# Performance work log

Measured on AMD Instinct MI355X. Metric: run time of the kernel, lower is better.

## Reference

```python
import jax, jax.numpy as jnp
import numpy as np

N = 100000        # nodes
E_RAND = 1600000  # random edges (self loops appended -> E = E_RAND + N)
H = 64            # agg_hidden
IN = 7            # in_channels
L = 3             # n_layer
FC = 128          # fc_hidden
C = 2             # num_classes
G = 256           # graphs in the batch
SLOPE = 0.2       # GATv2 LeakyReLU negative slope


def _gatv2(x, src, dst, Wl, bl, Wr, br, att, bias):
    # GATv2Conv, heads=1, concat=True, no edge_attr
    xl = x @ Wl.T + bl                                      # [N,H] source transform
    xr = x @ Wr.T + br                                      # [N,H] target transform
    e = jax.nn.leaky_relu(xl[src] + xr[dst], SLOPE) @ att   # [E] per-edge score
    m = jax.ops.segment_max(e, dst, num_segments=N)         # segment softmax over in-edges
    w = jnp.exp(e - m[dst])
    denom = jax.ops.segment_sum(w, dst, num_segments=N)
    alpha = w / denom[dst]                                  # self loops guarantee denom > 0
    out = jax.ops.segment_sum(alpha[:, None] * xl[src], dst, num_segments=N)
    return out + bias


def _forward(x, eps, m0, v0, mrest, vrest, fc1_W, fc1_b, fc2_W, fc2_b, edge_index, batch):
    src, dst = edge_index[0], edge_index[1]
    mean = jax.nn.elu(_gatv2(x, src, dst, *m0))
    log_var = jax.nn.elu(_gatv2(x, src, dst, *v0))
    for i in range(L - 1):  # dropout is a no-op in eval mode
        mean = jax.nn.elu(_gatv2(mean, src, dst, *[p[i] for p in mrest]))
        log_var = jax.nn.elu(_gatv2(log_var, src, dst, *[p[i] for p in vrest]))
    z = mean + eps * jnp.exp(0.5 * log_var)                 # reparameterize
    counts = jax.ops.segment_sum(jnp.ones((N,), z.dtype), batch, num_segments=G)
    zg = jax.ops.segment_sum(z, batch, num_segments=G) / counts[:, None]  # global_mean_pool
    h = jax.nn.relu(zg @ fc1_W.T + fc1_b)
    logits = h @ fc2_W.T + fc2_b
    return jax.nn.log_softmax(logits, axis=1), mean, log_var


def setup_inputs() -> dict:
    key = jax.random.key(0)
    ks = iter(jax.random.split(key, 48))

    def nrm(shape, s=0.1):
        return s * jax.random.normal(next(ks), shape, jnp.float32)

    x = jax.random.normal(next(ks), (N, IN), jnp.float32)
    src = jax.random.randint(next(ks), (E_RAND,), 0, N)
    dst = jax.random.randint(next(ks), (E_RAND,), 0, N)
    loops = jnp.arange(N)
    edge_index = jnp.stack([jnp.concatenate([src, loops]),
                            jnp.concatenate([dst, loops])])  # add_self_loops=True
    batch = jnp.sort(jax.random.randint(next(ks), (N,), 0, G))
    eps = jax.random.normal(next(ks), (N, H), jnp.float32)

    d = dict(x=x, eps=eps, edge_index=edge_index, batch=batch)
    for pre, din in (("m0", IN), ("v0", IN)):
        d[pre + "_Wl"] = nrm((H, din)); d[pre + "_bl"] = nrm((H,))
        d[pre + "_Wr"] = nrm((H, din)); d[pre + "_br"] = nrm((H,))
        d[pre + "_att"] = nrm((H,));    d[pre + "_bias"] = nrm((H,))
    for pre in ("m", "v"):  # stacked hidden layers [L-1, ...]
        d[pre + "_Wl"] = nrm((L - 1, H, H)); d[pre + "_bl"] = nrm((L - 1, H))
        d[pre + "_Wr"] = nrm((L - 1, H, H)); d[pre + "_br"] = nrm((L - 1, H))
        d[pre + "_att"] = nrm((L - 1, H));   d[pre + "_bias"] = nrm((L - 1, H))
    d["fc1_W"] = nrm((FC, H)); d["fc1_b"] = nrm((FC,))
    d["fc2_W"] = nrm((C, FC)); d["fc2_b"] = nrm((C,))
    return d


def reference(x, eps, edge_index, batch,
              m0_Wl, m0_bl, m0_Wr, m0_br, m0_att, m0_bias,
              v0_Wl, v0_bl, v0_Wr, v0_br, v0_att, v0_bias,
              m_Wl, m_bl, m_Wr, m_br, m_att, m_bias,
              v_Wl, v_bl, v_Wr, v_br, v_att, v_bias,
              fc1_W, fc1_b, fc2_W, fc2_b):
    m0 = (m0_Wl, m0_bl, m0_Wr, m0_br, m0_att, m0_bias)
    v0 = (v0_Wl, v0_bl, v0_Wr, v0_br, v0_att, v0_bias)
    mrest = (m_Wl, m_bl, m_Wr, m_br, m_att, m_bias)
    vrest = (v_Wl, v_bl, v_Wr, v_br, v_att, v_bias)
    return _forward(x, eps, m0, v0, mrest, vrest, fc1_W, fc1_b, fc2_W, fc2_b, edge_index, batch)
```

## Files before the change

### kernel.cpp

```cpp
#include <hip/hip_runtime.h>
#include <hip/hip_fp16.h>
#include <math.h>


#define BSH 7
#define BMSK ((1 << BSH) - 1)
#define CHUNK 4096
#define SNB 4096

typedef _Float16 h2 __attribute__((ext_vector_type(2)));
typedef _Float16 h8 __attribute__((ext_vector_type(8)));
typedef float f4 __attribute__((ext_vector_type(4)));

__device__ __forceinline__ float elu1(float v) {
    return v > 0.f ? v : (__expf(v) - 1.f);
}

__device__ __forceinline__ float exp2fast(float x) {
#if defined(__has_builtin)
#if __has_builtin(__builtin_amdgcn_exp2f)
    return __builtin_amdgcn_exp2f(x);
#else
    return exp2f(x);
#endif
#else
    return exp2f(x);
#endif
}

__device__ __forceinline__ float dot2f(h2 a, h2 b, float c) {
#if defined(__has_builtin)
#if __has_builtin(__builtin_amdgcn_fdot2)
    return __builtin_amdgcn_fdot2(a, b, c, false);
#else
    return fmaf((float)a.x, (float)b.x, fmaf((float)a.y, (float)b.y, c));
#endif
#else
    return fmaf((float)a.x, (float)b.x, fmaf((float)a.y, (float)b.y, c));
#endif
}

template <int CTRL>
__device__ __forceinline__ float dppf(float v) {
    int r = __builtin_amdgcn_update_dpp(0, __builtin_bit_cast(int, v), CTRL, 0xF, 0xF, true);
    return __builtin_bit_cast(float, r);
}


__global__ void k_hist_bucket(const int* __restrict__ dst, int E,
                              int* __restrict__ bcnt, int nbk) {
    __shared__ int h[1024];
    for (int i = threadIdx.x; i < 1024; i += blockDim.x) h[i] = 0;
    __syncthreads();
    int stride = gridDim.x * blockDim.x;
    for (int e = blockIdx.x * blockDim.x + threadIdx.x; e < E; e += stride)
        atomicAdd(&h[dst[e] >> BSH], 1);
    __syncthreads();
    for (int i = threadIdx.x; i < nbk; i += blockDim.x)
        if (h[i]) atomicAdd(&bcnt[i], h[i]);
}

__global__ void k_scan_buckets(const int* __restrict__ bcnt, int nbk, int* __restrict__ boff) {
    __shared__ int sh[1024];
    int t = threadIdx.x;
    int v = (t < nbk) ? bcnt[t] : 0;
    sh[t] = v;
    __syncthreads();
    for (int o = 1; o < 1024; o <<= 1) {
        int u = (t >= o) ? sh[t - o] : 0;
        __syncthreads();
        sh[t] += u;
        __syncthreads();
    }
    if (t < nbk) boff[t] = sh[t] - v;
    if (t == nbk - 1) boff[nbk] = sh[t];
}

__global__ __launch_bounds__(256) void k_binfill(
    const int* __restrict__ src, const int* __restrict__ dst, int E,
    const int* __restrict__ boff, int* __restrict__ bfill, int* __restrict__ pairs) {
    __shared__ int h[1024];
    __shared__ int sbase[1024];
    int c0 = blockIdx.x * CHUNK;
    int c1 = min(c0 + CHUNK, E);
    for (int i = threadIdx.x; i < 1024; i += 256) h[i] = 0;
    __syncthreads();
    for (int e = c0 + threadIdx.x; e < c1; e += 256)
        atomicAdd(&h[dst[e] >> BSH], 1);
    __syncthreads();
    for (int i = threadIdx.x; i < 1024; i += 256) {
        int c = h[i];
        sbase[i] = c ? (boff[i] + atomicAdd(&bfill[i], c)) : 0;
        h[i] = 0;
    }
    __syncthreads();
    for (int e = c0 + threadIdx.x; e < c1; e += 256) {
        int d = dst[e];
        int b = d >> BSH;
        int off = atomicAdd(&h[b], 1);
        pairs[sbase[b] + off] = (src[e] << BSH) | (d & BMSK);
    }
}

__global__ __launch_bounds__(256) void k_bucket_csr(
    const int* __restrict__ pairs, const int* __restrict__ boff,
    int* __restrict__ rowptr, int* __restrict__ col, int N, int E) {
    __shared__ int deg[128], fill[128], scan[128], base[128];
    int b = blockIdx.x;
    int e0 = boff[b], e1 = boff[b + 1];
    int t = threadIdx.x;
    if (t < 128) { deg[t] = 0; fill[t] = 0; }
    __syncthreads();
    for (int i = e0 + t; i < e1; i += 256)
        atomicAdd(&deg[pairs[i] & BMSK], 1);
    __syncthreads();
    if (t < 128) scan[t] = deg[t];
    __syncthreads();
    for (int o = 1; o < 128; o <<= 1) {
        int u = (t >= o && t < 128) ? scan[t - o] : 0;
        __syncthreads();
        if (t < 128) scan[t] += u;
        __syncthreads();
    }
    if (t < 128) {
        int excl = e0 + scan[t] - deg[t];
        int node = (b << BSH) + t;
        if (node < N) rowptr[node] = excl;
        if (node == N - 1) rowptr[N] = E;
        base[t] = excl;
    }
    __syncthreads();
    for (int i = e0 + t; i < e1; i += 256) {
        int pk = pairs[i];
        int d = pk & BMSK;
        int pos = base[d] + atomicAdd(&fill[d], 1);
        col[pos] = ((unsigned)pk) >> BSH;
    }
}


__global__ __launch_bounds__(256) void k_deg_hist(const int* __restrict__ rowptr, int n,
                                                  int* __restrict__ bin_cnt,
                                                  int* __restrict__ blk_base) {
    __shared__ int h[256];
    h[threadIdx.x] = 0;
    __syncthreads();
    int b0 = blockIdx.x * SNB;
    int b1 = min(b0 + SNB, n);
    for (int i = b0 + threadIdx.x; i < b1; i += 256) {
        int d = 255 - min(rowptr[i + 1] - rowptr[i], 255);
        atomicAdd(&h[d], 1);
    }
    __syncthreads();
    int c = h[threadIdx.x];
    blk_base[blockIdx.x * 256 + threadIdx.x] = c ? atomicAdd(&bin_cnt[threadIdx.x], c) : 0;
}

__global__ void k_scan256(const int* __restrict__ bin_cnt, int* __restrict__ bin_off) {
    __shared__ int sh[256];
    int t = threadIdx.x;
    int v = bin_cnt[t];
    sh[t] = v;
    __syncthreads();
    for (int o = 1; o < 256; o <<= 1) {
        int u = (t >= o) ? sh[t - o] : 0;
        __syncthreads();
        sh[t] += u;
        __syncthreads();
    }
    bin_off[t] = sh[t] - v;
}

__global__ __launch_bounds__(256) void k_deg_scatter(const int* __restrict__ rowptr, int n,
                                                     const int* __restrict__ bin_off,
                                                     const int* __restrict__ blk_base,
                                                     int* __restrict__ nodeof) {
    __shared__ int h[256];
    h[threadIdx.x] = 0;
    __syncthreads();
    int b0 = blockIdx.x * SNB;
    int b1 = min(b0 + SNB, n);
    for (int i = b0 + threadIdx.x; i < b1; i += 256) {
        int d = 255 - min(rowptr[i + 1] - rowptr[i], 255);
        int my = atomicAdd(&h[d], 1);
        nodeof[bin_off[d] + blk_base[blockIdx.x * 256 + d] + my] = i;
    }
}


__global__ void k_transform7(const float* __restrict__ X,
                             const float* __restrict__ mWl, const float* __restrict__ mbl,
                             const float* __restrict__ mWr, const float* __restrict__ mbr,
                             const float* __restrict__ vWl, const float* __restrict__ vbl,
                             const float* __restrict__ vWr, const float* __restrict__ vbr,
                             __half* __restrict__ xlb, __half* __restrict__ xrb, int n) {
    int t = blockIdx.x * blockDim.x + threadIdx.x;
    int node = t >> 6;
    if (node >= n) return;
    int h = t & 63;
    float aml = mbl[h], amr = mbr[h], avl = vbl[h], avr = vbr[h];
#pragma unroll
    for (int k = 0; k < 7; ++k) {
        float xv = X[node * 7 + k];
        aml = fmaf(xv, mWl[h * 7 + k], aml);
        amr = fmaf(xv, mWr[h * 7 + k], amr);
        avl = fmaf(xv, vWl[h * 7 + k], avl);
        avr = fmaf(xv, vWr[h * 7 + k], avr);
    }
    size_t o = (size_t)node * 128;
    xlb[o + h] = __float2half(aml);
    xlb[o + 64 + h] = __float2half(avl);
    xrb[o + h] = __float2half(amr);
    xrb[o + 64 + h] = __float2half(avr);
}

__global__ __launch_bounds__(256) void k_transform_mfma2(
    const float* __restrict__ Xm, const float* __restrict__ Xv,
    const float* __restrict__ mWl, const float* __restrict__ mbl,
    const float* __restrict__ mWr, const float* __restrict__ mbr,
    const float* __restrict__ vWl, const float* __restrict__ vbl,
    const float* __restrict__ vWr, const float* __restrict__ vbr,
    __half* __restrict__ xlb, __half* __restrict__ xrb, int n) {
    int brn = blockIdx.y;
    const float* X  = brn ? Xv : Xm;
    const float* Wl = brn ? vWl : mWl;
    const float* bl = brn ? vbl : mbl;
    const float* Wr = brn ? vWr : mWr;
    const float* br = brn ? vbr : mbr;
    int base = brn * 64;

    __shared__ float biasLds[128];
    {
        int t = threadIdx.x;
        if (t < 64) biasLds[t] = bl[t];
        else if (t < 128) biasLds[t] = br[t - 64];
    }
    __syncthreads();
    int lane = threadIdx.x & 63;
    int l16 = lane & 15, lhi = lane >> 4;

    h8 aW[2][8];
    const float* Wp0 = Wl + (size_t)l16 * 64 + lhi * 8;
    const float* Wp1 = Wr + (size_t)l16 * 64 + lhi * 8;
#pragma unroll
    for (int tl = 0; tl < 4; ++tl) {
#pragma unroll
        for (int c = 0; c < 2; ++c) {
            const float* p0 = Wp0 + (size_t)tl * 16 * 64 + c * 32;
            const float* p1 = Wp1 + (size_t)tl * 16 * 64 + c * 32;
            float4 u0 = *(const float4*)p0, u1 = *(const float4*)(p0 + 4);
            float4 v0 = *(const float4*)p1, v1 = *(const float4*)(p1 + 4);
            h8 a0 = {(_Float16)u0.x, (_Float16)u0.y, (_Float16)u0.z, (_Float16)u0.w,
                     (_Float16)u1.x, (_Float16)u1.y, (_Float16)u1.z, (_Float16)u1.w};
            h8 a1 = {(_Float16)v0.x, (_Float16)v0.y, (_Float16)v0.z, (_Float16)v0.w,
                     (_Float16)v1.x, (_Float16)v1.y, (_Float16)v1.z, (_Float16)v1.w};
            aW[0][tl * 2 + c] = a0;
            aW[1][tl * 2 + c] = a1;
        }
    }

    int ntiles = (n + 15) >> 4;
    int wtile = blockIdx.x * 4 + (threadIdx.x >> 6);
    int wstride = gridDim.x * 4;
    for (int tile = wtile; tile < ntiles; tile += wstride) {
        int nb = tile * 16;
        int node = nb + l16;
        int nload = min(node, n - 1);
        h8 Bf[2];
#pragma unroll
        for (int c = 0; c < 2; ++c) {
            const float* p = X + (size_t)nload * 64 + c * 32 + lhi * 8;
            float4 u0 = *(const float4*)p, u1 = *(const float4*)(p + 4);
            h8 b = {(_Float16)u0.x, (_Float16)u0.y, (_Float16)u0.z, (_Float16)u0.w,
                    (_Float16)u1.x, (_Float16)u1.y, (_Float16)u1.z, (_Float16)u1.w};
            Bf[c] = b;
        }
        f4 acc[2][4];
#pragma unroll
        for (int m = 0; m < 2; ++m)
#pragma unroll
            for (int tl = 0; tl < 4; ++tl) {
                f4 a = {0.f, 0.f, 0.f, 0.f};
                a = __builtin_amdgcn_mfma_f32_16x16x32_f16(aW[m][tl * 2 + 0], Bf[0], a, 0, 0, 0);
                a = __builtin_amdgcn_mfma_f32_16x16x32_f16(aW[m][tl * 2 + 1], Bf[1], a, 0, 0, 0);
                acc[m][tl] = a;
            }
        if (node < n) {
#pragma unroll
            for (int m = 0; m < 2; ++m) {
                __half* op = (m ? xrb : xlb) + (size_t)node * 128 + base;
#pragma unroll
                for (int tl = 0; tl < 4; ++tl) {
                    float4 bb = *(const float4*)&biasLds[m * 64 + tl * 16 + 4 * lhi];
                    h2 lo = {(_Float16)(acc[m][tl][0] + bb.x), (_Float16)(acc[m][tl][1] + bb.y)};
                    h2 hi = {(_Float16)(acc[m][tl][2] + bb.z), (_Float16)(acc[m][tl][3] + bb.w)};
                    uint2 pk = {*(unsigned*)&lo, *(unsigned*)&hi};
                    *(uint2*)(op + tl * 16 + 4 * lhi) = pk;
                }
            }
        }
    }
}


__global__ __launch_bounds__(256) void k_aggregate2(
    const __half* __restrict__ xlb, const __half* __restrict__ xrb,
    const float* __restrict__ attm, const float* __restrict__ attv,
    const float* __restrict__ biasm, const float* __restrict__ biasv,
    const int* __restrict__ rowptr, const int* __restrict__ col,
    const int* __restrict__ nodeof,
    float* __restrict__ outm, float* __restrict__ outv, int n) {
    int t = blockIdx.x * blockDim.x + threadIdx.x;
    int gid = t >> 4;
    if (gid >= n) return;
    int node = nodeof[gid];
    int l = t & 15;
    int s = l & 7;
    bool isv = l >= 8;

    int4 xri = ((const int4*)(xrb + (size_t)node * 128))[l];
    h2 xr0 = *(h2*)&xri.x, xr1 = *(h2*)&xri.y, xr2 = *(h2*)&xri.z, xr3 = *(h2*)&xri.w;
    const float* ap = (isv ? attv : attm) + s * 8;
    float4 af0 = *(const float4*)ap, af1 = *(const float4*)(ap + 4);
    const float C6 = 0.6f * 1.44269504f;
    const float C4 = 0.4f * 1.44269504f;
    h2 a6_0 = {(_Float16)(af0.x * C6), (_Float16)(af0.y * C6)};
    h2 a6_1 = {(_Float16)(af0.z * C6), (_Float16)(af0.w * C6)};
    h2 a6_2 = {(_Float16)(af1.x * C6), (_Float16)(af1.y * C6)};
    h2 a6_3 = {(_Float16)(af1.z * C6), (_Float16)(af1.w * C6)};
    h2 a4_0 = {(_Float16)(af0.x * C4), (_Float16)(af0.y * C4)};
    h2 a4_1 = {(_Float16)(af0.z * C4), (_Float16)(af0.w * C4)};
    h2 a4_2 = {(_Float16)(af1.x * C4), (_Float16)(af1.y * C4)};
    h2 a4_3 = {(_Float16)(af1.z * C4), (_Float16)(af1.w * C4)};

    float ac0 = 0.f, ac1 = 0.f, ac2 = 0.f, ac3 = 0.f;
    float ac4 = 0.f, ac5 = 0.f, ac6 = 0.f, ac7 = 0.f;
    float ssum = 0.f;

    auto proc = [&](int4 qi) {
        h2 x0 = *(h2*)&qi.x, x1 = *(h2*)&qi.y, x2 = *(h2*)&qi.z, x3 = *(h2*)&qi.w;
        h2 y0 = x0 + xr0, y1 = x1 + xr1, y2 = x2 + xr2, y3 = x3 + xr3;
        int z0i = (*(int*)&y0) & 0x7FFF7FFF;
        int z1i = (*(int*)&y1) & 0x7FFF7FFF;
        int z2i = (*(int*)&y2) & 0x7FFF7FFF;
        int z3i = (*(int*)&y3) & 0x7FFF7FFF;
        h2 z0 = *(h2*)&z0i, z1 = *(h2*)&z1i, z2 = *(h2*)&z2i, z3 = *(h2*)&z3i;
        float sc = dot2f(y0, a6_0, 0.f);
        float sa = dot2f(z0, a4_0, 0.f);
        sc = dot2f(y1, a6_1, sc);
        sa = dot2f(z1, a4_1, sa);
        sc = dot2f(y2, a6_2, sc);
        sa = dot2f(z2, a4_2, sa);
        sc = dot2f(y3, a6_3, sc);
        sa = dot2f(z3, a4_3, sa);
        sc += sa;
        sc += dppf<0xB1>(sc);
        sc += dppf<0x4E>(sc);
        sc += dppf<0x141>(sc);
        float w = exp2fast(sc);
        ssum += w;
        ac0 = fmaf(w, (float)x0.x, ac0);
        ac1 = fmaf(w, (float)x0.y, ac1);
        ac2 = fmaf(w, (float)x1.x, ac2);
        ac3 = fmaf(w, (float)x1.y, ac3);
        ac4 = fmaf(w, (float)x2.x, ac4);
        ac5 = fmaf(w, (float)x2.y, ac5);
        ac6 = fmaf(w, (float)x3.x, ac6);
        ac7 = fmaf(w, (float)x3.y, ac7);
    };

    int r0 = rowptr[node], r1 = rowptr[node + 1];
    const int4* xp = (const int4*)xlb + l;
    int last = r1 - 1;
    int nb = (r1 - r0) >> 2;
    int e = r0;
    int t0 = 0, t1 = 0, t2 = 0, t3 = 0;
    int4 qA0, qA1, qA2, qA3;
    if (nb) {
        int s0 = col[e], s1 = col[e + 1], s2 = col[e + 2], s3 = col[e + 3];
        qA0 = xp[(size_t)s0 * 16]; qA1 = xp[(size_t)s1 * 16];
        qA2 = xp[(size_t)s2 * 16]; qA3 = xp[(size_t)s3 * 16];
        int p = e + 4;
        t0 = col[min(p, last)];     t1 = col[min(p + 1, last)];
        t2 = col[min(p + 2, last)]; t3 = col[min(p + 3, last)];
    }
    for (int b = 0; b < nb; ++b) {
        int4 qB0, qB1, qB2, qB3;
        bool more = (b + 1 < nb);
        if (more) {
            qB0 = xp[(size_t)t0 * 16]; qB1 = xp[(size_t)t1 * 16];
            qB2 = xp[(size_t)t2 * 16]; qB3 = xp[(size_t)t3 * 16];
            int p = e + 8;
            t0 = col[min(p, last)];     t1 = col[min(p + 1, last)];
            t2 = col[min(p + 2, last)]; t3 = col[min(p + 3, last)];
        }
        proc(qA0); proc(qA1); proc(qA2); proc(qA3);
        if (more) { qA0 = qB0; qA1 = qB1; qA2 = qB2; qA3 = qB3; }
        e += 4;
    }
    for (e = r0 + nb * 4; e < r1; ++e)
        proc(xp[(size_t)col[e] * 16]);

    float inv = 1.f / ssum;
    const float* bp = (isv ? biasv : biasm) + s * 8;
    float4 b0 = *(const float4*)bp, b1 = *(const float4*)(bp + 4);
    float* op = (isv ? outv : outm) + (size_t)node * 64 + s * 8;
    float4 r0v, r1v;
    r0v.x = elu1(fmaf(ac0, inv, b0.x));
    r0v.y = elu1(fmaf(ac1, inv, b0.y));
    r0v.z = elu1(fmaf(ac2, inv, b0.z));
    r0v.w = elu1(fmaf(ac3, inv, b0.w));
    r1v.x = elu1(fmaf(ac4, inv, b1.x));
    r1v.y = elu1(fmaf(ac5, inv, b1.y));
    r1v.z = elu1(fmaf(ac6, inv, b1.z));
    r1v.w = elu1(fmaf(ac7, inv, b1.w));
    *(float4*)op = r0v;
    *(float4*)(op + 4) = r1v;
}


__global__ void k_zpool(const float* __restrict__ mean, const float* __restrict__ logvar,
                        const float* __restrict__ eps, const int* __restrict__ batch,
                        float* __restrict__ zsum, float* __restrict__ cnt, int n) {
    int wave = blockIdx.x * 4 + (threadIdx.x >> 6);
    int lane = threadIdx.x & 63;
    int n0 = wave * 16;
    if (n0 >= n) return;
    int n1 = min(n0 + 16, n);
    float acc = 0.f, c = 0.f;
    int gcur = -1;
    for (int nd = n0; nd < n1; ++nd) {
        int g = batch[nd];
        if (g != gcur) {
            if (gcur >= 0) {
                atomicAdd(&zsum[gcur * 64 + lane], acc);
                if (lane == 0) atomicAdd(&cnt[gcur], c);
            }
            gcur = g; acc = 0.f; c = 0.f;
        }
        size_t o = (size_t)nd * 64 + lane;
        float z = fmaf(eps[o], __expf(0.5f * logvar[o]), mean[o]);
        acc += z;
        c += 1.f;
    }
    if (gcur >= 0) {
        atomicAdd(&zsum[gcur * 64 + lane], acc);
        if (lane == 0) atomicAdd(&cnt[gcur], c);
    }
}


__global__ void k_fchead(const float* __restrict__ zsum, const float* __restrict__ cnt,
                         const float* __restrict__ fc1W, const float* __restrict__ fc1b,
                         const float* __restrict__ fc2W, const float* __restrict__ fc2b,
                         float* __restrict__ out) {
    __shared__ float zg[64];
    __shared__ float h1[128];
    __shared__ float lg[2];
    int g = blockIdx.x;
    int t = threadIdx.x;
    if (t < 64) zg[t] = zsum[g * 64 + t] / cnt[g];
    __syncthreads();
    float h = fc1b[t];
#pragma unroll
    for (int k = 0; k < 64; ++k) h = fmaf(zg[k], fc1W[t * 64 + k], h);
    h1[t] = fmaxf(h, 0.f);
    __syncthreads();
    if (t < 2) {
        float l = fc2b[t];
        for (int k = 0; k < 128; ++k) l = fmaf(h1[k], fc2W[t * 128 + k], l);
        lg[t] = l;
    }
    __syncthreads();
    if (t == 0) {
        float mx = fmaxf(lg[0], lg[1]);
        float lse = mx + logf(expf(lg[0] - mx) + expf(lg[1] - mx));
        out[g * 2 + 0] = lg[0] - lse;
        out[g * 2 + 1] = lg[1] - lse;
    }
}


extern "C" void kernel_launch(void* const* d_in, const int* in_sizes, int n_in,
                              void* d_out, int out_size, void* d_ws, size_t ws_size,
                              hipStream_t stream) {
    const float* x     = (const float*)d_in[0];
    const float* eps   = (const float*)d_in[1];
    const int*   eidx  = (const int*)d_in[2];
    const int*   batch = (const int*)d_in[3];
    const float* m0_Wl = (const float*)d_in[4];
    const float* m0_bl = (const float*)d_in[5];
    const float* m0_Wr = (const float*)d_in[6];
    const float* m0_br = (const float*)d_in[7];
    const float* m0_att = (const float*)d_in[8];
    const float* m0_bias = (const float*)d_in[9];
    const float* v0_Wl = (const float*)d_in[10];
    const float* v0_bl = (const float*)d_in[11];
    const float* v0_Wr = (const float*)d_in[12];
    const float* v0_br = (const float*)d_in[13];
    const float* v0_att = (const float*)d_in[14];
    const float* v0_bias = (const float*)d_in[15];
    const float* m_Wl = (const float*)d_in[16];
    const float* m_bl = (const float*)d_in[17];
    const float* m_Wr = (const float*)d_in[18];
    const float* m_br = (const float*)d_in[19];
    const float* m_att = (const float*)d_in[20];
    const float* m_bias = (const float*)d_in[21];
    const float* v_Wl = (const float*)d_in[22];
    const float* v_bl = (const float*)d_in[23];
    const float* v_Wr = (const float*)d_in[24];
    const float* v_br = (const float*)d_in[25];
    const float* v_att = (const float*)d_in[26];
    const float* v_bias = (const float*)d_in[27];
    const float* fc1W = (const float*)d_in[28];
    const float* fc1b = (const float*)d_in[29];
    const float* fc2W = (const float*)d_in[30];
    const float* fc2b = (const float*)d_in[31];

    const int N = in_sizes[1] / 64;
    const int E = in_sizes[2] / 2;
    const int G = (out_size - N * 128) / 2;
    const int nbk = (N + (1 << BSH) - 1) >> BSH;
    const int nsb = (N + SNB - 1) / SNB;
    const int* srcp = eidx;
    const int* dstp = eidx + E;

    char* wsb = (char*)d_ws;
    size_t off = 0;
    auto carve = [&](size_t bytes) -> void* {
        void* p = wsb + off;
        off += (bytes + 255) & ~(size_t)255;
        return p;
    };
    int*    rowptr   = (int*)carve((size_t)(N + 1) * sizeof(int));
    int*    col      = (int*)carve((size_t)E * sizeof(int));
    int*    pairs    = (int*)carve((size_t)E * sizeof(int));
    int*    bcnt     = (int*)carve((size_t)(nbk + 1) * sizeof(int));
    int*    boff     = (int*)carve((size_t)(nbk + 1) * sizeof(int));
    int*    bfill    = (int*)carve((size_t)nbk * sizeof(int));
    int*    nodeof   = (int*)carve((size_t)N * sizeof(int));
    int*    bin_cnt  = (int*)carve(256 * sizeof(int));
    int*    bin_off  = (int*)carve(256 * sizeof(int));
    int*    blk_base = (int*)carve((size_t)nsb * 256 * sizeof(int));
    __half* xlb      = (__half*)carve((size_t)N * 128 * sizeof(__half));
    __half* xrb      = (__half*)carve((size_t)N * 128 * sizeof(__half));
    float*  zsum     = (float*)carve((size_t)G * 64 * sizeof(float));
    float*  cnt      = (float*)carve((size_t)G * sizeof(float));
    (void)ws_size;

    float* out_logits = (float*)d_out;
    float* mean_buf   = out_logits + (size_t)G * 2;
    float* logvar_buf = mean_buf + (size_t)N * 64;

    const int agrid = (N * 16 + 255) / 256;
    const int tgrid7 = (N * 64 + 255) / 256;
    const int mgrid = ((N + 15) / 16 + 3) / 4;
    const int zgrid = ((N + 15) / 16 + 3) / 4;

    (void)hipMemsetAsync(bcnt, 0, (size_t)nbk * sizeof(int), stream);
    (void)hipMemsetAsync(bfill, 0, (size_t)nbk * sizeof(int), stream);
    (void)hipMemsetAsync(bin_cnt, 0, 256 * sizeof(int), stream);
    (void)hipMemsetAsync(zsum, 0, (size_t)G * 64 * sizeof(float), stream);
    (void)hipMemsetAsync(cnt, 0, (size_t)G * sizeof(float), stream);
    k_hist_bucket<<<256, 256, 0, stream>>>(dstp, E, bcnt, nbk);
    k_scan_buckets<<<1, 1024, 0, stream>>>(bcnt, nbk, boff);
    k_binfill<<<(E + CHUNK - 1) / CHUNK, 256, 0, stream>>>(srcp, dstp, E, boff, bfill, pairs);
    k_bucket_csr<<<nbk, 256, 0, stream>>>(pairs, boff, rowptr, col, N, E);

    k_deg_hist<<<nsb, 256, 0, stream>>>(rowptr, N, bin_cnt, blk_base);
    k_scan256<<<1, 256, 0, stream>>>(bin_cnt, bin_off);
    k_deg_scatter<<<nsb, 256, 0, stream>>>(rowptr, N, bin_off, blk_base, nodeof);

    k_transform7<<<tgrid7, 256, 0, stream>>>(x, m0_Wl, m0_bl, m0_Wr, m0_br,
                                             v0_Wl, v0_bl, v0_Wr, v0_br, xlb, xrb, N);
    k_aggregate2<<<agrid, 256, 0, stream>>>(xlb, xrb, m0_att, v0_att, m0_bias, v0_bias,
                                            rowptr, col, nodeof, mean_buf, logvar_buf, N);

    for (int l = 0; l < 2; ++l) {
        k_transform_mfma2<<<dim3(mgrid, 2), 256, 0, stream>>>(
            mean_buf, logvar_buf,
            m_Wl + (size_t)l * 4096, m_bl + l * 64, m_Wr + (size_t)l * 4096, m_br + l * 64,
            v_Wl + (size_t)l * 4096, v_bl + l * 64, v_Wr + (size_t)l * 4096, v_br + l * 64,
            xlb, xrb, N);
        k_aggregate2<<<agrid, 256, 0, stream>>>(xlb, xrb, m_att + l * 64, v_att + l * 64,
                                                m_bias + l * 64, v_bias + l * 64,
                                                rowptr, col, nodeof, mean_buf, logvar_buf, N);
    }

    k_zpool<<<zgrid, 256, 0, stream>>>(mean_buf, logvar_buf, eps, batch, zsum, cnt, N);
    k_fchead<<<G, 128, 0, stream>>>(zsum, cnt, fc1W, fc1b, fc2W, fc2b, out_logits);
}
```

Baseline: 485.0 us.

## Fuse degree sort, memsets and z-pooling into existing kernels

```diff
diff --git a/kernel.cpp b/kernel.cpp
--- a/kernel.cpp
+++ b/kernel.cpp
@@ -60,9 +60,12 @@
         if (h[i]) atomicAdd(&bcnt[i], h[i]);
 }
 
-__global__ void k_scan_buckets(const int* __restrict__ bcnt, int nbk, int* __restrict__ boff) {
+__global__ void k_scan_buckets(const int* __restrict__ bcnt, int nbk, int* __restrict__ boff,
+                               int* __restrict__ bfill, int* __restrict__ bin_cnt) {
     __shared__ int sh[1024];
     int t = threadIdx.x;
+    if (t < nbk) bfill[t] = 0;
+    if (t < 256) bin_cnt[t] = 0;
     int v = (t < nbk) ? bcnt[t] : 0;
     sh[t] = v;
     __syncthreads();
@@ -104,7 +107,8 @@
 
 __global__ __launch_bounds__(256) void k_bucket_csr(
     const int* __restrict__ pairs, const int* __restrict__ boff,
-    int* __restrict__ rowptr, int* __restrict__ col, int N, int E) {
+    int* __restrict__ rowptr, int* __restrict__ col,
+    int* __restrict__ bin_cnt, int* __restrict__ keytick, int N, int E) {
     __shared__ int deg[128], fill[128], scan[128], base[128];
     int b = blockIdx.x;
     int e0 = boff[b], e1 = boff[b + 1];
@@ -125,7 +129,12 @@
     if (t < 128) {
         int excl = e0 + scan[t] - deg[t];
         int node = (b << BSH) + t;
-        if (node < N) rowptr[node] = excl;
+        if (node < N) {
+            rowptr[node] = excl;
+            int key = 255 - min(deg[t], 255);
+            int tick = atomicAdd(&bin_cnt[key], 1);
+            keytick[node] = (key << 24) | tick;
+        }
         if (node == N - 1) rowptr[N] = E;
         base[t] = excl;
     }
@@ -138,27 +147,11 @@
     }
 }
 
-
-__global__ __launch_bounds__(256) void k_deg_hist(const int* __restrict__ rowptr, int n,
-                                                  int* __restrict__ bin_cnt,
-                                                  int* __restrict__ blk_base) {
-    __shared__ int h[256];
-    h[threadIdx.x] = 0;
-    __syncthreads();
-    int b0 = blockIdx.x * SNB;
-    int b1 = min(b0 + SNB, n);
-    for (int i = b0 + threadIdx.x; i < b1; i += 256) {
-        int d = 255 - min(rowptr[i + 1] - rowptr[i], 255);
-        atomicAdd(&h[d], 1);
-    }
-    __syncthreads();
-    int c = h[threadIdx.x];
-    blk_base[blockIdx.x * 256 + threadIdx.x] = c ? atomicAdd(&bin_cnt[threadIdx.x], c) : 0;
-}
-
-__global__ void k_scan256(const int* __restrict__ bin_cnt, int* __restrict__ bin_off) {
+__global__ void k_scan256(const int* __restrict__ bin_cnt, int* __restrict__ bin_off,
+                          float* __restrict__ zsum, int G) {
     __shared__ int sh[256];
     int t = threadIdx.x;
+    for (int i = t; i < G * 64; i += 256) zsum[i] = 0.f;
     int v = bin_cnt[t];
     sh[t] = v;
     __syncthreads();
@@ -171,20 +164,13 @@
     bin_off[t] = sh[t] - v;
 }
 
-__global__ __launch_bounds__(256) void k_deg_scatter(const int* __restrict__ rowptr, int n,
+__global__ __launch_bounds__(256) void k_key_scatter(const int* __restrict__ keytick,
                                                      const int* __restrict__ bin_off,
-                                                     const int* __restrict__ blk_base,
-                                                     int* __restrict__ nodeof) {
-    __shared__ int h[256];
-    h[threadIdx.x] = 0;
-    __syncthreads();
-    int b0 = blockIdx.x * SNB;
-    int b1 = min(b0 + SNB, n);
-    for (int i = b0 + threadIdx.x; i < b1; i += 256) {
-        int d = 255 - min(rowptr[i + 1] - rowptr[i], 255);
-        int my = atomicAdd(&h[d], 1);
-        nodeof[bin_off[d] + blk_base[blockIdx.x * 256 + d] + my] = i;
-    }
+                                                     int* __restrict__ nodeof, int n) {
+    int i = blockIdx.x * 256 + threadIdx.x;
+    if (i >= n) return;
+    int kt = keytick[i];
+    nodeof[bin_off[((unsigned)kt) >> 24] + (kt & 0xFFFFFF)] = i;
 }
 
 
@@ -303,13 +289,16 @@
 }
 
 
+template <bool FUSE>
 __global__ __launch_bounds__(256) void k_aggregate2(
     const __half* __restrict__ xlb, const __half* __restrict__ xrb,
     const float* __restrict__ attm, const float* __restrict__ attv,
     const float* __restrict__ biasm, const float* __restrict__ biasv,
     const int* __restrict__ rowptr, const int* __restrict__ col,
     const int* __restrict__ nodeof,
-    float* __restrict__ outm, float* __restrict__ outv, int n) {
+    float* __restrict__ outm, float* __restrict__ outv, int n,
+    const float* __restrict__ eps, const int* __restrict__ batch,
+    float* __restrict__ zsum) {
     int t = blockIdx.x * blockDim.x + threadIdx.x;
     int gid = t >> 4;
     if (gid >= n) return;
@@ -416,50 +405,52 @@
     r1v.w = elu1(fmaf(ac7, inv, b1.w));
     *(float4*)op = r0v;
     *(float4*)(op + 4) = r1v;
-}
-
-
-__global__ void k_zpool(const float* __restrict__ mean, const float* __restrict__ logvar,
-                        const float* __restrict__ eps, const int* __restrict__ batch,
-                        float* __restrict__ zsum, float* __restrict__ cnt, int n) {
-    int wave = blockIdx.x * 4 + (threadIdx.x >> 6);
-    int lane = threadIdx.x & 63;
-    int n0 = wave * 16;
-    if (n0 >= n) return;
-    int n1 = min(n0 + 16, n);
-    float acc = 0.f, c = 0.f;
-    int gcur = -1;
-    for (int nd = n0; nd < n1; ++nd) {
-        int g = batch[nd];
-        if (g != gcur) {
-            if (gcur >= 0) {
-                atomicAdd(&zsum[gcur * 64 + lane], acc);
-                if (lane == 0) atomicAdd(&cnt[gcur], c);
-            }
-            gcur = g; acc = 0.f; c = 0.f;
-        }
-        size_t o = (size_t)nd * 64 + lane;
-        float z = fmaf(eps[o], __expf(0.5f * logvar[o]), mean[o]);
-        acc += z;
-        c += 1.f;
-    }
-    if (gcur >= 0) {
-        atomicAdd(&zsum[gcur * 64 + lane], acc);
-        if (lane == 0) atomicAdd(&cnt[gcur], c);
-    }
-}
-
-
-__global__ void k_fchead(const float* __restrict__ zsum, const float* __restrict__ cnt,
+
+    if (FUSE) {
+        float lv0 = __shfl_xor(r0v.x, 8), lv1 = __shfl_xor(r0v.y, 8);
+        float lv2 = __shfl_xor(r0v.z, 8), lv3 = __shfl_xor(r0v.w, 8);
+        float lv4 = __shfl_xor(r1v.x, 8), lv5 = __shfl_xor(r1v.y, 8);
+        float lv6 = __shfl_xor(r1v.z, 8), lv7 = __shfl_xor(r1v.w, 8);
+        if (!isv) {
+            int g = batch[node];
+            const float* ep = eps + (size_t)node * 64 + s * 8;
+            float4 e0 = *(const float4*)ep, e1 = *(const float4*)(ep + 4);
+            float* zp = zsum + (size_t)g * 64 + s * 8;
+            atomicAdd(zp + 0, fmaf(e0.x, __expf(0.5f * lv0), r0v.x));
+            atomicAdd(zp + 1, fmaf(e0.y, __expf(0.5f * lv1), r0v.y));
+            atomicAdd(zp + 2, fmaf(e0.z, __expf(0.5f * lv2), r0v.z));
+            atomicAdd(zp + 3, fmaf(e0.w, __expf(0.5f * lv3), r0v.w));
+            atomicAdd(zp + 4, fmaf(e1.x, __expf(0.5f * lv4), r1v.x));
+            atomicAdd(zp + 5, fmaf(e1.y, __expf(0.5f * lv5), r1v.y));
+            atomicAdd(zp + 6, fmaf(e1.z, __expf(0.5f * lv6), r1v.z));
+            atomicAdd(zp + 7, fmaf(e1.w, __expf(0.5f * lv7), r1v.w));
+        }
+    }
+}
+
+
+__global__ void k_fchead(const float* __restrict__ zsum, const int* __restrict__ batch,
+                         int N,
                          const float* __restrict__ fc1W, const float* __restrict__ fc1b,
                          const float* __restrict__ fc2W, const float* __restrict__ fc2b,
                          float* __restrict__ out) {
     __shared__ float zg[64];
     __shared__ float h1[128];
     __shared__ float lg[2];
+    __shared__ int bnd[2];
     int g = blockIdx.x;
     int t = threadIdx.x;
-    if (t < 64) zg[t] = zsum[g * 64 + t] / cnt[g];
+    if (t < 2) {
+        int tgt = g + t, lo = 0, hi = N;
+        while (lo < hi) {
+            int m = (lo + hi) >> 1;
+            if (batch[m] < tgt) lo = m + 1; else hi = m;
+        }
+        bnd[t] = lo;
+    }
+    __syncthreads();
+    float cntg = (float)(bnd[1] - bnd[0]);
+    if (t < 64) zg[t] = zsum[g * 64 + t] / cntg;
     __syncthreads();
     float h = fc1b[t];
 #pragma unroll
@@ -521,7 +512,6 @@
     const int E = in_sizes[2] / 2;
     const int G = (out_size - N * 128) / 2;
     const int nbk = (N + (1 << BSH) - 1) >> BSH;
-    const int nsb = (N + SNB - 1) / SNB;
     const int* srcp = eidx;
     const int* dstp = eidx + E;
 
@@ -539,13 +529,12 @@
     int*    boff     = (int*)carve((size_t)(nbk + 1) * sizeof(int));
     int*    bfill    = (int*)carve((size_t)nbk * sizeof(int));
     int*    nodeof   = (int*)carve((size_t)N * sizeof(int));
+    int*    keytick  = (int*)carve((size_t)N * sizeof(int));
     int*    bin_cnt  = (int*)carve(256 * sizeof(int));
     int*    bin_off  = (int*)carve(256 * sizeof(int));
-    int*    blk_base = (int*)carve((size_t)nsb * 256 * sizeof(int));
     __half* xlb      = (__half*)carve((size_t)N * 128 * sizeof(__half));
     __half* xrb      = (__half*)carve((size_t)N * 128 * sizeof(__half));
     float*  zsum     = (float*)carve((size_t)G * 64 * sizeof(float));
-    float*  cnt      = (float*)carve((size_t)G * sizeof(float));
     (void)ws_size;
 
     float* out_logits = (float*)d_out;
@@ -555,26 +544,21 @@
     const int agrid = (N * 16 + 255) / 256;
     const int tgrid7 = (N * 64 + 255) / 256;
     const int mgrid = ((N + 15) / 16 + 3) / 4;
-    const int zgrid = ((N + 15) / 16 + 3) / 4;
 
     (void)hipMemsetAsync(bcnt, 0, (size_t)nbk * sizeof(int), stream);
-    (void)hipMemsetAsync(bfill, 0, (size_t)nbk * sizeof(int), stream);
-    (void)hipMemsetAsync(bin_cnt, 0, 256 * sizeof(int), stream);
-    (void)hipMemsetAsync(zsum, 0, (size_t)G * 64 * sizeof(float), stream);
-    (void)hipMemsetAsync(cnt, 0, (size_t)G * sizeof(float), stream);
     k_hist_bucket<<<256, 256, 0, stream>>>(dstp, E, bcnt, nbk);
-    k_scan_buckets<<<1, 1024, 0, stream>>>(bcnt, nbk, boff);
+    k_scan_buckets<<<1, 1024, 0, stream>>>(bcnt, nbk, boff, bfill, bin_cnt);
     k_binfill<<<(E + CHUNK - 1) / CHUNK, 256, 0, stream>>>(srcp, dstp, E, boff, bfill, pairs);
-    k_bucket_csr<<<nbk, 256, 0, stream>>>(pairs, boff, rowptr, col, N, E);
-
-    k_deg_hist<<<nsb, 256, 0, stream>>>(rowptr, N, bin_cnt, blk_base);
-    k_scan256<<<1, 256, 0, stream>>>(bin_cnt, bin_off);
-    k_deg_scatter<<<nsb, 256, 0, stream>>>(rowptr, N, bin_off, blk_base, nodeof);
+    k_bucket_csr<<<nbk, 256, 0, stream>>>(pairs, boff, rowptr, col, bin_cnt, keytick, N, E);
+
+    k_scan256<<<1, 256, 0, stream>>>(bin_cnt, bin_off, zsum, G);
+    k_key_scatter<<<(N + 255) / 256, 256, 0, stream>>>(keytick, bin_off, nodeof, N);
 
     k_transform7<<<tgrid7, 256, 0, stream>>>(x, m0_Wl, m0_bl, m0_Wr, m0_br,
                                              v0_Wl, v0_bl, v0_Wr, v0_br, xlb, xrb, N);
-    k_aggregate2<<<agrid, 256, 0, stream>>>(xlb, xrb, m0_att, v0_att, m0_bias, v0_bias,
-                                            rowptr, col, nodeof, mean_buf, logvar_buf, N);
+    k_aggregate2<false><<<agrid, 256, 0, stream>>>(xlb, xrb, m0_att, v0_att, m0_bias, v0_bias,
+                                                   rowptr, col, nodeof, mean_buf, logvar_buf, N,
+                                                   nullptr, nullptr, nullptr);
 
     for (int l = 0; l < 2; ++l) {
         k_transform_mfma2<<<dim3(mgrid, 2), 256, 0, stream>>>(
@@ -582,11 +566,15 @@
             m_Wl + (size_t)l * 4096, m_bl + l * 64, m_Wr + (size_t)l * 4096, m_br + l * 64,
             v_Wl + (size_t)l * 4096, v_bl + l * 64, v_Wr + (size_t)l * 4096, v_br + l * 64,
             xlb, xrb, N);
-        k_aggregate2<<<agrid, 256, 0, stream>>>(xlb, xrb, m_att + l * 64, v_att + l * 64,
-                                                m_bias + l * 64, v_bias + l * 64,
-                                                rowptr, col, nodeof, mean_buf, logvar_buf, N);
-    }
-
-    k_zpool<<<zgrid, 256, 0, stream>>>(mean_buf, logvar_buf, eps, batch, zsum, cnt, N);
-    k_fchead<<<G, 128, 0, stream>>>(zsum, cnt, fc1W, fc1b, fc2W, fc2b, out_logits);
-}
+        if (l == 0)
+            k_aggregate2<false><<<agrid, 256, 0, stream>>>(
+                xlb, xrb, m_att + l * 64, v_att + l * 64, m_bias + l * 64, v_bias + l * 64,
+                rowptr, col, nodeof, mean_buf, logvar_buf, N, nullptr, nullptr, nullptr);
+        else
+            k_aggregate2<true><<<agrid, 256, 0, stream>>>(
+                xlb, xrb, m_att + l * 64, v_att + l * 64, m_bias + l * 64, v_bias + l * 64,
+                rowptr, col, nodeof, mean_buf, logvar_buf, N, eps, batch, zsum);
+    }
+
+    k_fchead<<<G, 128, 0, stream>>>(zsum, batch, N, fc1W, fc1b, fc2W, fc2b, out_logits);
+}
```

After: 954.3 us. 1.97x slower.
